# Performance work log

Hardware: AMD Instinct MI355X
Metric: run time of the kernel (lower is better)

The kernel has to match this reference:

```python
import jax, jax.numpy as jnp
import numpy as np

B, T, D = 8, 2048, 1024
N_CONCEPTS = 4096


def setup_inputs() -> dict:
    key = jax.random.key(0)
    k1, k2 = jax.random.split(key)
    x = jax.random.normal(k1, (B, T, D), dtype=jnp.float32)
    embedding = jax.random.normal(k2, (N_CONCEPTS, D), dtype=jnp.float32)
    return {"x": x, "embedding": embedding}


def reference(x, embedding):
    # x: [B, T, D]; embedding (codebook): [K, D]
    Bb, Tt, Dd = x.shape
    x_flat = x.reshape(Bb * Tt, Dd)                      # [N, D]
    distances = (
        jnp.sum(x_flat * x_flat, axis=1, keepdims=True)
        - 2.0 * jnp.einsum("nd,kd->nk", x_flat, embedding)
        + jnp.sum(embedding * embedding, axis=1)
    )
    encoding_indices = jnp.argmin(distances, axis=1)     # [N]
    # one_hot @ embedding in the original is exactly a row gather
    quantized = embedding[encoding_indices]              # [N, D]
    # straight-through estimator
    quantized = x_flat + jax.lax.stop_gradient(quantized - x_flat)
    return quantized.reshape(Bb, Tt, Dd)
```

## Files before the change

### kernel.cpp

```cpp
#include <hip/hip_runtime.h>


#define NROWS 16384
#define DDIM  1024
#define KCB   4096
#define MARGIN 1.0f

typedef _Float16 f16x8 __attribute__((ext_vector_type(8)));
typedef float    f32x4 __attribute__((ext_vector_type(4)));

__global__ __launch_bounds__(256) void enorm_kernel(const float* __restrict__ e,
                                                    float* __restrict__ enorm) {
    const int k = blockIdx.x;
    const int tid = threadIdx.x;
    const float4 v = reinterpret_cast<const float4*>(e + (size_t)k * DDIM)[tid];
    double a = (double)v.x * v.x + (double)v.y * v.y + (double)v.z * v.z + (double)v.w * v.w;
    __shared__ double sm[256];
    sm[tid] = a;
    __syncthreads();
    for (int s = 128; s > 0; s >>= 1) {
        if (tid < s) sm[tid] += sm[tid + s];
        __syncthreads();
    }
    if (tid == 0) enorm[k] = (float)sm[0];
}

__global__ __launch_bounds__(256) void cvt16_kernel(const float* __restrict__ in,
                                                    _Float16* __restrict__ out, int n8) {
    const int i = blockIdx.x * 256 + threadIdx.x;
    if (i >= n8) return;
    const float4 a = reinterpret_cast<const float4*>(in)[2 * i];
    const float4 b = reinterpret_cast<const float4*>(in)[2 * i + 1];
    f16x8 h;
    h[0] = (_Float16)a.x; h[1] = (_Float16)a.y; h[2] = (_Float16)a.z; h[3] = (_Float16)a.w;
    h[4] = (_Float16)b.x; h[5] = (_Float16)b.y; h[6] = (_Float16)b.z; h[7] = (_Float16)b.w;
    reinterpret_cast<f16x8*>(out)[i] = h;
}

__device__ __forceinline__ void gld_lds16(const void* g, void* l) {
    __builtin_amdgcn_global_load_lds(
        (const __attribute__((address_space(1))) unsigned int*)g,
        (__attribute__((address_space(3))) unsigned int*)l,
        16, 0, 0);
}

__device__ __forceinline__ void top2_merge(float& b1, int& i1, float& b2, int& i2,
                                           float c1, int j1, float c2, int j2) {
    if (c1 < b1 || (c1 == b1 && j1 < i1)) {
        float nb2; int ni2;
        if (b1 < c2 || (b1 == c2 && i1 < j2)) { nb2 = b1; ni2 = i1; }
        else { nb2 = c2; ni2 = j2; }
        b2 = nb2; i2 = ni2; b1 = c1; i1 = j1;
    } else if (c1 < b2 || (c1 == b2 && j1 < i2)) {
        b2 = c1; i2 = j1;
    }
}

__global__ __launch_bounds__(256, 2) void mfma_top2_kernel(
    const _Float16* __restrict__ xh, const _Float16* __restrict__ eh,
    const float* __restrict__ enorm,
    float* __restrict__ ps, int* __restrict__ pi) {

    __shared__ __align__(16) _Float16 s_x[128 * 64];
    __shared__ __align__(16) _Float16 s_e[128 * 64];
    __shared__ float s_ens[128];
    __shared__ float s_rs[128][2][2];
    __shared__ int   s_ri[128][2][2];

    const int tid = threadIdx.x;
    const int l   = tid & 63;
    const int w   = tid >> 6;
    const int wr  = w >> 1;
    const int wc  = w & 1;
    const int n0  = blockIdx.y * 128;
    const int k0  = blockIdx.x * 128;

    if (tid < 128) s_ens[tid] = enorm[k0 + tid];

    const int srow = l >> 3;
    const int scol = ((l & 7) ^ (l >> 3)) * 8;
    const int arow = wr * 64 + (l & 15);
    const int brow = wc * 64 + (l & 15);
    const int g    = l >> 4;

    f32x4 acc[4][4];
    #pragma unroll
    for (int m = 0; m < 4; ++m)
        #pragma unroll
        for (int n = 0; n < 4; ++n)
            acc[m][n] = (f32x4)0.f;

    const char* cx = (const char*)s_x;
    const char* ce = (const char*)s_e;

    for (int d0 = 0; d0 < DDIM; d0 += 64) {
        #pragma unroll
        for (int i = 0; i < 4; ++i) {
            const int rb = (w * 4 + i) * 8;
            gld_lds16(xh + (size_t)(n0 + rb + srow) * DDIM + d0 + scol,
                      (void*)(s_x + (w * 4 + i) * 512));
            gld_lds16(eh + (size_t)(k0 + rb + srow) * DDIM + d0 + scol,
                      (void*)(s_e + (w * 4 + i) * 512));
        }
        __syncthreads();

        #pragma unroll
        for (int ks = 0; ks < 2; ++ks) {
            const int ph = (((ks * 4 + g) ^ (l & 7)) << 4);
            f16x8 a[4], b[4];
            #pragma unroll
            for (int m = 0; m < 4; ++m)
                a[m] = *(const f16x8*)(cx + (arow + m * 16) * 128 + ph);
            #pragma unroll
            for (int n = 0; n < 4; ++n)
                b[n] = *(const f16x8*)(ce + (brow + n * 16) * 128 + ph);
            #pragma unroll
            for (int m = 0; m < 4; ++m)
                #pragma unroll
                for (int n = 0; n < 4; ++n)
                    acc[m][n] = __builtin_amdgcn_mfma_f32_16x16x32_f16(a[m], b[n], acc[m][n], 0, 0, 0);
        }
        __syncthreads();
    }

    #pragma unroll
    for (int m = 0; m < 4; ++m) {
        #pragma unroll
        for (int reg = 0; reg < 4; ++reg) {
            float b1 = 3.4e38f, b2 = 3.4e38f;
            int   i1 = 0x7fffffff, i2 = 0x7fffffff;
            #pragma unroll
            for (int n = 0; n < 4; ++n) {
                const int cl = wc * 64 + n * 16 + (l & 15);
                const float s = fmaf(-2.f, acc[m][n][reg], s_ens[cl]);
                const int ki = k0 + cl;
                if (s < b1 || (s == b1 && ki < i1)) { b2 = b1; i2 = i1; b1 = s; i1 = ki; }
                else if (s < b2 || (s == b2 && ki < i2)) { b2 = s; i2 = ki; }
            }
            #pragma unroll
            for (int d = 1; d < 16; d <<= 1) {
                const float c1 = __shfl_xor(b1, d); const int j1 = __shfl_xor(i1, d);
                const float c2 = __shfl_xor(b2, d); const int j2 = __shfl_xor(i2, d);
                top2_merge(b1, i1, b2, i2, c1, j1, c2, j2);
            }
            if ((l & 15) == 0) {
                const int R = wr * 64 + m * 16 + (l >> 4) * 4 + reg;
                s_rs[R][wc][0] = b1; s_ri[R][wc][0] = i1;
                s_rs[R][wc][1] = b2; s_ri[R][wc][1] = i2;
            }
        }
    }
    __syncthreads();
    if (tid < 128) {
        float b1 = s_rs[tid][0][0], b2 = s_rs[tid][0][1];
        int   i1 = s_ri[tid][0][0], i2 = s_ri[tid][0][1];
        top2_merge(b1, i1, b2, i2,
                   s_rs[tid][1][0], s_ri[tid][1][0],
                   s_rs[tid][1][1], s_ri[tid][1][1]);
        const size_t o0 = (size_t)(blockIdx.x * 2 + 0) * NROWS + n0 + tid;
        const size_t o1 = (size_t)(blockIdx.x * 2 + 1) * NROWS + n0 + tid;
        ps[o0] = b1; pi[o0] = i1;
        ps[o1] = b2; pi[o1] = i2;
    }
}

__global__ __launch_bounds__(256) void refine_gather_kernel(
    const float* __restrict__ x, const float* __restrict__ e,
    const float* __restrict__ ps, const int* __restrict__ pi,
    float* __restrict__ out) {
    const int n = blockIdx.x;
    const int tid = threadIdx.x;
    __shared__ int s_cand[8];
    __shared__ int s_ncand;
    __shared__ double s_red[256];

    if (tid < 64) {
        const float s = ps[(size_t)tid * NROWS + n];
        const int  ki = pi[(size_t)tid * NROWS + n];
        float mn = s;
        #pragma unroll
        for (int d = 1; d < 64; d <<= 1) mn = fminf(mn, __shfl_xor(mn, d));
        const bool cand = (s <= mn + MARGIN);
        const unsigned long long bal = __ballot(cand);
        if (tid == 0) s_ncand = (int)__popcll(bal);
        if (cand) {
            const int r = (int)__popcll(bal & ((1ull << tid) - 1ull));
            if (r < 8) s_cand[r] = ki;
        }
    }
    __syncthreads();
    int nc = s_ncand;
    int bi;
    if (nc == 1) {
        bi = s_cand[0];
    } else {
        if (nc > 8) nc = 8;
        const float4 xv = *reinterpret_cast<const float4*>(x + (size_t)n * DDIM + tid * 4);
        double bs = 1e300;
        int bidx = 0x7fffffff;
        for (int c = 0; c < nc; ++c) {
            const int ki = s_cand[c];
            const float4 ev = *reinterpret_cast<const float4*>(e + (size_t)ki * DDIM + tid * 4);
            double p = 0.0;
            p += (double)ev.x * ev.x - 2.0 * (double)xv.x * ev.x;
            p += (double)ev.y * ev.y - 2.0 * (double)xv.y * ev.y;
            p += (double)ev.z * ev.z - 2.0 * (double)xv.z * ev.z;
            p += (double)ev.w * ev.w - 2.0 * (double)xv.w * ev.w;
            s_red[tid] = p;
            __syncthreads();
            for (int st = 128; st > 0; st >>= 1) {
                if (tid < st) s_red[tid] += s_red[tid + st];
                __syncthreads();
            }
            const double sc = s_red[0];
            __syncthreads();
            if (sc < bs || (sc == bs && ki < bidx)) { bs = sc; bidx = ki; }
        }
        bi = bidx;
    }
    const float4* src = reinterpret_cast<const float4*>(e + (size_t)bi * DDIM);
    reinterpret_cast<float4*>(out + (size_t)n * DDIM)[tid] = src[tid];
}

#define BN 128
#define BK 128
#define BD 16
#define KSPLIT 4
#define KPER (KCB / KSPLIT)

__global__ __launch_bounds__(256) void argmin_kernel(const float* __restrict__ x,
                                                     const float* __restrict__ e,
                                                     const float* __restrict__ enorm,
                                                     float* __restrict__ ps,
                                                     int* __restrict__ pi) {
    __shared__ float xs[BD][BN];
    __shared__ float es[BD][BK];
    __shared__ float ens[BK];
    __shared__ float rs[BN][17];
    __shared__ int   ri[BN][17];

    const int tid = threadIdx.x;
    const int tx = tid & 15;
    const int ty = tid >> 4;
    const int n0 = blockIdx.x * BN;
    const int kbase = blockIdx.y * KPER;

    float best[8];
    int   bidx[8];
    #pragma unroll
    for (int m = 0; m < 8; ++m) { best[m] = 3.4e38f; bidx[m] = 0x7fffffff; }

    for (int kt = 0; kt < KPER; kt += BK) {
        const int k0 = kbase + kt;
        __syncthreads();
        if (tid < BK) ens[tid] = enorm[k0 + tid];

        float acc[8][8];
        #pragma unroll
        for (int m = 0; m < 8; ++m)
            #pragma unroll
            for (int q = 0; q < 8; ++q) acc[m][q] = 0.f;

        for (int d0 = 0; d0 < DDIM; d0 += BD) {
            #pragma unroll
            for (int r = 0; r < 2; ++r) {
                const int j = tid + r * 256;
                const int row = j >> 2;
                const int c = (j & 3) << 2;
                const float4 v = *reinterpret_cast<const float4*>(
                    x + (size_t)(n0 + row) * DDIM + d0 + c);
                xs[c + 0][row] = v.x; xs[c + 1][row] = v.y;
                xs[c + 2][row] = v.z; xs[c + 3][row] = v.w;
            }
            #pragma unroll
            for (int r = 0; r < 2; ++r) {
                const int j = tid + r * 256;
                const int row = j >> 2;
                const int c = (j & 3) << 2;
                const float4 v = *reinterpret_cast<const float4*>(
                    e + (size_t)(k0 + row) * DDIM + d0 + c);
                es[c + 0][row] = v.x; es[c + 1][row] = v.y;
                es[c + 2][row] = v.z; es[c + 3][row] = v.w;
            }
            __syncthreads();
            #pragma unroll
            for (int d = 0; d < BD; ++d) {
                const float4 xa = *reinterpret_cast<const float4*>(&xs[d][ty * 8]);
                const float4 xb = *reinterpret_cast<const float4*>(&xs[d][ty * 8 + 4]);
                const float4 ea = *reinterpret_cast<const float4*>(&es[d][tx * 8]);
                const float4 eb = *reinterpret_cast<const float4*>(&es[d][tx * 8 + 4]);
                const float xv[8] = {xa.x, xa.y, xa.z, xa.w, xb.x, xb.y, xb.z, xb.w};
                const float ev[8] = {ea.x, ea.y, ea.z, ea.w, eb.x, eb.y, eb.z, eb.w};
                #pragma unroll
                for (int m = 0; m < 8; ++m)
                    #pragma unroll
                    for (int q = 0; q < 8; ++q)
                        acc[m][q] = fmaf(xv[m], ev[q], acc[m][q]);
            }
            __syncthreads();
        }

        #pragma unroll
        for (int m = 0; m < 8; ++m) {
            #pragma unroll
            for (int q = 0; q < 8; ++q) {
                const float s = fmaf(-2.f, acc[m][q], ens[tx * 8 + q]);
                const int ki = k0 + tx * 8 + q;
                if (s < best[m]) { best[m] = s; bidx[m] = ki; }
            }
        }
    }

    #pragma unroll
    for (int m = 0; m < 8; ++m) {
        rs[ty * 8 + m][tx] = best[m];
        ri[ty * 8 + m][tx] = bidx[m];
    }
    __syncthreads();
    if (tid < BN) {
        float bs = rs[tid][0];
        int   bi = ri[tid][0];
        #pragma unroll
        for (int t = 1; t < 16; ++t) {
            const float s  = rs[tid][t];
            const int   i2 = ri[tid][t];
            if (s < bs || (s == bs && i2 < bi)) { bs = s; bi = i2; }
        }
        ps[(size_t)blockIdx.y * NROWS + n0 + tid] = bs;
        pi[(size_t)blockIdx.y * NROWS + n0 + tid] = bi;
    }
}

__global__ __launch_bounds__(256) void merge_gather_kernel(const float* __restrict__ e,
                                                           const float* __restrict__ ps,
                                                           const int* __restrict__ pi,
                                                           float* __restrict__ out) {
    const int n = blockIdx.x;
    float bs = ps[n];
    int   bi = pi[n];
    #pragma unroll
    for (int h = 1; h < KSPLIT; ++h) {
        const float s  = ps[(size_t)h * NROWS + n];
        const int   i2 = pi[(size_t)h * NROWS + n];
        if (s < bs || (s == bs && i2 < bi)) { bs = s; bi = i2; }
    }
    const float4* src = reinterpret_cast<const float4*>(e + (size_t)bi * DDIM);
    float4* dst = reinterpret_cast<float4*>(out + (size_t)n * DDIM);
    dst[threadIdx.x] = src[threadIdx.x];
}

extern "C" void kernel_launch(void* const* d_in, const int* in_sizes, int n_in,
                              void* d_out, int out_size, void* d_ws, size_t ws_size,
                              hipStream_t stream) {
    const float* x = (const float*)d_in[0];
    const float* e = (const float*)d_in[1];
    float* out = (float*)d_out;
    char* ws = (char*)d_ws;

    const size_t MB = 1024 * 1024;
    const size_t need = 56 * MB;

    if (ws_size >= need) {
        float*    enorm = (float*)(ws);
        float*    ps    = (float*)(ws + 1 * MB);
        int*      pi    = (int*)  (ws + 6 * MB);
        _Float16* xh    = (_Float16*)(ws + 16 * MB);
        _Float16* ehp   = (_Float16*)(ws + 48 * MB);

        enorm_kernel<<<KCB, 256, 0, stream>>>(e, enorm);
        cvt16_kernel<<<(NROWS * DDIM / 8 + 255) / 256, 256, 0, stream>>>(x, xh, NROWS * DDIM / 8);
        cvt16_kernel<<<(KCB * DDIM / 8 + 255) / 256, 256, 0, stream>>>(e, ehp, KCB * DDIM / 8);
        mfma_top2_kernel<<<dim3(KCB / 128, NROWS / 128), 256, 0, stream>>>(
            xh, ehp, enorm, ps, pi);
        refine_gather_kernel<<<NROWS, 256, 0, stream>>>(x, e, ps, pi, out);
    } else {
        float* enorm = (float*)ws;
        float* ps    = (float*)(ws + 16 * 1024);
        int*   pi    = (int*)(ws + 16 * 1024 + KSPLIT * NROWS * 4);

        enorm_kernel<<<KCB, 256, 0, stream>>>(e, enorm);
        argmin_kernel<<<dim3(NROWS / BN, KSPLIT), 256, 0, stream>>>(x, e, enorm, ps, pi);
        merge_gather_kernel<<<NROWS, 256, 0, stream>>>(e, ps, pi, out);
    }
}
```

Measured before the change: 511.5 us.

## Double-buffer LDS tiles to overlap global loads with MFMA compute

Splits the x and codebook LDS tiles into two buffers and issues the global-to-LDS loads for the next 64-wide D slice before computing on the current one, so there is one barrier per iteration instead of two. The aim is to hide global load latency behind the MFMA work. It doubles LDS use to about 64KB per block, which may limit the two-blocks-per-CU occupancy, and it relies on the single barrier being enough for the direct-to-LDS loads to complete.

```diff
diff --git a/kernel.cpp b/kernel.cpp
--- a/kernel.cpp
+++ b/kernel.cpp
@@ -61,8 +61,8 @@
     const float* __restrict__ enorm,
     float* __restrict__ ps, int* __restrict__ pi) {
 
-    __shared__ __align__(16) _Float16 s_x[128 * 64];
-    __shared__ __align__(16) _Float16 s_e[128 * 64];
+    __shared__ __align__(16) _Float16 s_x[2][128 * 64];
+    __shared__ __align__(16) _Float16 s_e[2][128 * 64];
     __shared__ float s_ens[128];
     __shared__ float s_rs[128][2][2];
     __shared__ int   s_ri[128][2][2];
@@ -90,20 +90,23 @@
         for (int n = 0; n < 4; ++n)
             acc[m][n] = (f32x4)0.f;
 
-    const char* cx = (const char*)s_x;
-    const char* ce = (const char*)s_e;
-
-    for (int d0 = 0; d0 < DDIM; d0 += 64) {
+    const size_t xbase = (size_t)(n0 + srow) * DDIM + scol;
+    const size_t ebase = (size_t)(k0 + srow) * DDIM + scol;
+
+    auto STAGE = [&](int buf, int d0) {
         #pragma unroll
         for (int i = 0; i < 4; ++i) {
             const int rb = (w * 4 + i) * 8;
-            gld_lds16(xh + (size_t)(n0 + rb + srow) * DDIM + d0 + scol,
-                      (void*)(s_x + (w * 4 + i) * 512));
-            gld_lds16(eh + (size_t)(k0 + rb + srow) * DDIM + d0 + scol,
-                      (void*)(s_e + (w * 4 + i) * 512));
-        }
-        __syncthreads();
-
+            gld_lds16(xh + xbase + (size_t)rb * DDIM + d0,
+                      (void*)(s_x[buf] + (w * 4 + i) * 512));
+            gld_lds16(eh + ebase + (size_t)rb * DDIM + d0,
+                      (void*)(s_e[buf] + (w * 4 + i) * 512));
+        }
+    };
+
+    auto COMPUTE = [&](int buf) {
+        const char* cx = (const char*)s_x[buf];
+        const char* ce = (const char*)s_e[buf];
         #pragma unroll
         for (int ks = 0; ks < 2; ++ks) {
             const int ph = (((ks * 4 + g) ^ (l & 7)) << 4);
@@ -120,8 +123,18 @@
                 for (int n = 0; n < 4; ++n)
                     acc[m][n] = __builtin_amdgcn_mfma_f32_16x16x32_f16(a[m], b[n], acc[m][n], 0, 0, 0);
         }
+    };
+
+    STAGE(0, 0);
+    __syncthreads();
+    int cur = 0;
+    for (int t = 0; t < 15; ++t) {
+        STAGE(cur ^ 1, (t + 1) * 64);
+        COMPUTE(cur);
         __syncthreads();
-    }
+        cur ^= 1;
+    }
+    COMPUTE(cur);
 
     #pragma unroll
     for (int m = 0; m < 4; ++m) {
```

Measured after the change: 579.6 us. +13.3%, slower.
